# Optimization experiments

Hardware: AMD Instinct MI355X
Metric: run time of the kernel (lower is better)

The kernel has to match this reference:

```python
import jax, jax.numpy as jnp
import numpy as np

B, D, T = 16, 256, 4096
K = 1024
COMMITMENT_COST = 0.25


def setup_inputs() -> dict:
    key = jax.random.key(0)
    k1, k2 = jax.random.split(key)
    z = jax.random.normal(k1, (B, D, T), dtype=jnp.float32)
    # codebook initialized uniform(-1/K, 1/K) as in the torch module
    embeddings = jax.random.uniform(k2, (K, D), dtype=jnp.float32,
                                    minval=-1.0 / K, maxval=1.0 / K)
    return {"z": z, "embeddings": embeddings}


def reference(z, embeddings):
    # z: (B, D, T) -> (B, T, D)
    zt = jnp.transpose(z, (0, 2, 1))
    flat_z = zt.reshape(-1, D)  # (N, D), N = B*T
    # squared L2 distances to every codebook entry: (N, K)
    distances = (jnp.sum(flat_z * flat_z, axis=1, keepdims=True)
                 + jnp.sum(embeddings * embeddings, axis=1)
                 - 2.0 * flat_z @ embeddings.T)
    indices = jnp.argmin(distances, axis=1)  # (N,)
    # gather replaces the one-hot @ embeddings matmul (same result)
    quantized = embeddings[indices].reshape(B, T, D)
    # commitment loss (quantized detached)
    e_latent_loss = jnp.mean((jax.lax.stop_gradient(quantized) - zt) ** 2)
    loss = COMMITMENT_COST * e_latent_loss
    # straight-through estimator
    quantized_ste = zt + jax.lax.stop_gradient(quantized - zt)
    # perplexity from mean of one-hot encodings = normalized code histogram
    counts = jnp.zeros((K,), dtype=jnp.float32).at[indices].add(1.0)
    avg_probs = counts / flat_z.shape[0]
    perplexity = jnp.exp(-jnp.sum(avg_probs * jnp.log(avg_probs + 1e-10)))
    out = jnp.transpose(quantized_ste, (0, 2, 1))  # (B, D, T)
    return out, indices.reshape(B, T), loss, perplexity
```

## Files before the change

kernel.cpp:

```cpp
#include <hip/hip_runtime.h>
#include <hip/hip_bf16.h>

#define BB 16
#define DDIM 256
#define TLEN 4096
#define KCODES 1024
#define NQ (BB*TLEN)
#define QB 64
#define MAXC 32

#define FLT_MAX_C 3.402823466e+38f

using short8 = __attribute__((ext_vector_type(8))) short;
using f32x4  = __attribute__((ext_vector_type(4))) float;

__device__ __forceinline__ unsigned short f2bf(float x) {
  unsigned u = __float_as_uint(x);
  unsigned r = (u + 0x7fffu + ((u >> 16) & 1u)) >> 16;
  return (unsigned short)r;
}

__device__ __forceinline__ float np_sumsq_128(const float* q, int stride) {
  float r[8];
#pragma unroll
  for (int j = 0; j < 8; ++j) {
    float v = q[(size_t)j * (size_t)stride];
    r[j] = __fmul_rn(v, v);
  }
  for (int i = 8; i < 128; i += 8) {
#pragma unroll
    for (int j = 0; j < 8; ++j) {
      float v = q[(size_t)(i + j) * (size_t)stride];
      r[j] = __fadd_rn(r[j], __fmul_rn(v, v));
    }
  }
  return __fadd_rn(__fadd_rn(__fadd_rn(r[0], r[1]), __fadd_rn(r[2], r[3])),
                   __fadd_rn(__fadd_rn(r[4], r[5]), __fadd_rn(r[6], r[7])));
}
__device__ __forceinline__ float np_sumsq_256s(const float* p, int stride) {
  return __fadd_rn(np_sumsq_128(p, stride),
                   np_sumsq_128(p + (size_t)128 * stride, stride));
}

__global__ void k_prep(const float* __restrict__ emb, float* __restrict__ e2,
                       short* __restrict__ ebh, unsigned* __restrict__ maxe) {
  const int k = blockIdx.x;
  const int d = threadIdx.x;
  __shared__ float row[DDIM];
  float v = emb[(size_t)k * DDIM + d];
  row[d] = v;
  ebh[(size_t)k * DDIM + d] = (short)f2bf(v);
  float a = fabsf(v);
#pragma unroll
  for (int m = 1; m < 64; m <<= 1) a = fmaxf(a, __shfl_xor(a, m, 64));
  if ((threadIdx.x & 63) == 0) atomicMax(maxe, __float_as_uint(a));
  __syncthreads();
  if (d == 0) e2[k] = np_sumsq_256s(row, 1);
}

__global__ __launch_bounds__(512, 1)
void k_mdist(const float* __restrict__ z, const float* __restrict__ emb,
             const short* __restrict__ ebh, const float* __restrict__ e2,
             const unsigned* __restrict__ maxeU, float* __restrict__ out,
             float* __restrict__ oidx, int* __restrict__ hist,
             double* __restrict__ lossp) {
  extern __shared__ __align__(16) char sbuf[];
  float*  zf   = (float*)sbuf;
  short8* abh  = (short8*)(sbuf + 65536);
  float* bd    = (float*)(sbuf + 65536);
  int*   bk    = (int*)(sbuf + 65536 + 2048);
  float* sm    = (float*)(sbuf + 98304);
  float* qmin  = (float*)(sbuf + 98304 + 2048);
  int*   cand  = (int*)(sbuf + 98304 + 2304);
  int*   cnt   = (int*)(sbuf + 98304 + 10496);
  int*   ovf   = (int*)(sbuf + 98304 + 10752);
  float* z2s   = (float*)(sbuf + 98304 + 11008);
  float* sabs  = (float*)(sbuf + 98304 + 11264);
  int*   sidxs = (int*)(sbuf + 98304 + 11520);

  const int tid = threadIdx.x;
  const int lane = tid & 63;
  const int w = tid >> 6;
  const int g = lane >> 4;
  const int c = lane & 15;
  const int n0 = blockIdx.x * QB;
  const int b = n0 >> 12;
  const int t0 = n0 & (TLEN - 1);
  const float* zp = z + (size_t)b * DDIM * TLEN + t0;

#pragma unroll
  for (int i = 0; i < 8; ++i) {
    int s4 = i * 512 + tid;
    int dl = s4 >> 4, q4 = (s4 & 15) * 4;
    *(float4*)&zf[dl * QB + q4] = *(const float4*)(zp + (size_t)dl * TLEN + q4);
  }
  __syncthreads();

#pragma unroll
  for (int i = 0; i < 4; ++i) {
    int s = i * 512 + tid;
    int ks = s >> 8, mt = (s >> 6) & 3, ln = s & 63;
    int q = mt * 16 + (ln & 15);
    int d0 = ks * 32 + (ln >> 4) * 8;
    short8 hh;
#pragma unroll
    for (int j = 0; j < 8; ++j) hh[j] = (short)f2bf(zf[(d0 + j) * QB + q]);
    abh[s] = hh;
  }
  if (tid < QB) {
    z2s[tid] = np_sumsq_256s(&zf[tid], QB);
    float sa = 0.f;
    for (int d = 0; d < DDIM; ++d) sa += fabsf(zf[d * QB + tid]);
    sabs[tid] = sa;
    cnt[tid] = 0;
    ovf[tid] = 0;
  }
  __syncthreads();

  const float maxe = __uint_as_float(*maxeU);

#pragma unroll 1
  for (int h = 0; h < 2; ++h) {
    const int kb = h * 512 + w * 64;

    f32x4 acc[4][4];
#pragma unroll
    for (int mt = 0; mt < 4; ++mt)
#pragma unroll
      for (int nt = 0; nt < 4; ++nt) {
        f32x4 zz = {0.f, 0.f, 0.f, 0.f};
        acc[mt][nt] = zz;
      }

    const short* ebp = ebh + (size_t)(kb + c) * DDIM + g * 8;
    short8 bbuf[4];
#pragma unroll
    for (int nt = 0; nt < 4; ++nt)
      bbuf[nt] = *(const short8*)(ebp + nt * (16 * DDIM));

    for (int ks = 0; ks < 8; ++ks) {
      short8 ah[4];
#pragma unroll
      for (int mt = 0; mt < 4; ++mt) ah[mt] = abh[ks * 256 + mt * 64 + lane];
      const int ksn = (ks + 1) & 7;
#pragma unroll
      for (int nt = 0; nt < 4; ++nt) {
        short8 bv = bbuf[nt];
        bbuf[nt] = *(const short8*)(ebp + nt * (16 * DDIM) + ksn * 32);
#pragma unroll
        for (int mt = 0; mt < 4; ++mt)
          acc[mt][nt] = __builtin_amdgcn_mfma_f32_16x16x32_bf16(
              ah[mt], bv, acc[mt][nt], 0, 0, 0);
      }
    }

    float e2c[4];
#pragma unroll
    for (int nt = 0; nt < 4; ++nt) e2c[nt] = e2[kb + nt * 16 + c];

#pragma unroll
    for (int mt = 0; mt < 4; ++mt) {
      float m4[4];
#pragma unroll
      for (int r = 0; r < 4; ++r) {
        float m = FLT_MAX_C;
#pragma unroll
        for (int nt = 0; nt < 4; ++nt)
          m = fminf(m, e2c[nt] - 2.0f * acc[mt][nt][r]);
#pragma unroll
        for (int s = 1; s < 16; s <<= 1) m = fminf(m, __shfl_xor(m, s, 64));
        m4[r] = m;
      }
      if (c == 0) {
#pragma unroll
        for (int r = 0; r < 4; ++r) sm[w * 64 + mt * 16 + g * 4 + r] = m4[r];
      }
    }
    __syncthreads();
    if (tid < QB) {
      float m = sm[tid];
#pragma unroll
      for (int wv = 1; wv < 8; ++wv) m = fminf(m, sm[wv * 64 + tid]);
      qmin[tid] = m;
    }
    __syncthreads();

#pragma unroll
    for (int mt = 0; mt < 4; ++mt)
#pragma unroll
      for (int r = 0; r < 4; ++r) {
        const int ql = mt * 16 + g * 4 + r;
        const float lim = qmin[ql] + (maxe * sabs[ql]) * 0.016f + 2e-4f;
#pragma unroll
        for (int nt = 0; nt < 4; ++nt) {
          float s = e2c[nt] - 2.0f * acc[mt][nt][r];
          if (s <= lim) {
            int p = atomicAdd(&cnt[ql], 1);
            if (p < MAXC) cand[ql * MAXC + p] = kb + nt * 16 + c;
            else ovf[ql] = 1;
          }
        }
      }
    __syncthreads();
  }

  {
    const int q = tid & 63;
    const int slot = tid >> 6;
    const float z2q = z2s[q];
    float bestd = FLT_MAX_C;
    int besti = (1 << 30);
    const bool all = (ovf[q] != 0) || (cnt[q] > MAXC);
    const int count = all ? KCODES : cnt[q];
    for (int ci = slot; ci < count; ci += 8) {
      const int k = all ? ci : cand[q * MAXC + ci];
      const float4* ek = (const float4*)(emb + (size_t)k * DDIM);
      float a0 = 0.f;
      for (int dd = 0; dd < 64; ++dd) {
        float4 e4 = ek[dd];
        a0 = __fmaf_rn(zf[(dd * 4 + 0) * QB + q], e4.x, a0);
        a0 = __fmaf_rn(zf[(dd * 4 + 1) * QB + q], e4.y, a0);
        a0 = __fmaf_rn(zf[(dd * 4 + 2) * QB + q], e4.z, a0);
        a0 = __fmaf_rn(zf[(dd * 4 + 3) * QB + q], e4.w, a0);
      }
      float dist = __fsub_rn(__fadd_rn(z2q, e2[k]), __fmul_rn(2.0f, a0));
      if (dist < bestd || (dist == bestd && k < besti)) { bestd = dist; besti = k; }
    }
    bd[q * 8 + slot] = bestd;
    bk[q * 8 + slot] = besti;
  }
  __syncthreads();

  if (tid < QB) {
    float B = bd[tid * 8 + 0];
    int K = bk[tid * 8 + 0];
#pragma unroll
    for (int s = 1; s < 8; ++s) {
      float d2 = bd[tid * 8 + s];
      int k2 = bk[tid * 8 + s];
      if (d2 < B || (d2 == B && k2 < K)) { B = d2; K = k2; }
    }
    K &= (KCODES - 1);
    sidxs[tid] = K;
    oidx[n0 + tid] = (float)K;
    atomicAdd(&hist[K], 1);
    double ls = (double)B;
#pragma unroll
    for (int m = 1; m < 64; m <<= 1) ls += __shfl_xor(ls, m, 64);
    if (tid == 0) lossp[blockIdx.x] = ls;
  }
  __syncthreads();

  float* obase = out + (size_t)b * DDIM * TLEN + t0;
#pragma unroll
  for (int i = 0; i < 32; ++i) {
    int e = i * 512 + tid;
    int q = e & 63, d = e >> 6;
    obase[(size_t)d * TLEN + q] = emb[(size_t)sidxs[q] * DDIM + d];
  }
}

__global__ void k_final(const int* __restrict__ hist,
                        const double* __restrict__ lossp,
                        float* __restrict__ out2) {
  const int tid = threadIdx.x;
  double ls = 0.0;
  for (int i = 0; i < 4; ++i) ls += lossp[tid * 4 + i];
  float es = 0.f;
  for (int i = tid; i < KCODES; i += 256) {
    float p = (float)hist[i] / 65536.0f;
    es += p * logf(p + 1e-10f);
  }
#pragma unroll
  for (int m = 1; m < 64; m <<= 1) {
    ls += __shfl_xor(ls, m, 64);
    es += __shfl_xor(es, m, 64);
  }
  __shared__ double lw[4];
  __shared__ float ew[4];
  if ((tid & 63) == 0) { lw[tid >> 6] = ls; ew[tid >> 6] = es; }
  __syncthreads();
  if (tid == 0) {
    double lt = lw[0] + lw[1] + lw[2] + lw[3];
    float et = ew[0] + ew[1] + ew[2] + ew[3];
    float loss = 0.25f * (float)(lt / (double)((long long)NQ * DDIM));
    float perp = expf(-et);
    out2[0] = loss;
    out2[1] = perp;
  }
}

extern "C" void kernel_launch(void* const* d_in, const int* in_sizes, int n_in,
                              void* d_out, int out_size, void* d_ws, size_t ws_size,
                              hipStream_t stream) {
  const float* z = (const float*)d_in[0];
  const float* emb = (const float*)d_in[1];
  float* out = (float*)d_out;

  char* ws = (char*)d_ws;
  float* e2 = (float*)(ws);
  int* hist = (int*)(ws + 4096);
  unsigned* maxe = (unsigned*)(ws + 8192);
  double* lossp = (double*)(ws + 8200);
  short* ebh = (short*)(ws + 16400);

  float* oidx = out + ((size_t)out_size - 2 - NQ);
  float* out2 = out + ((size_t)out_size - 2);

  (void)hipFuncSetAttribute((const void*)k_mdist,
                            hipFuncAttributeMaxDynamicSharedMemorySize,
                            110080);

  hipMemsetAsync(hist, 0, 4100, stream);

  k_prep<<<KCODES, 256, 0, stream>>>(emb, e2, ebh, maxe);
  k_mdist<<<NQ / QB, 512, 110080, stream>>>(z, emb, ebh, e2, maxe, out, oidx,
                                            hist, lossp);
  k_final<<<1, 256, 0, stream>>>(hist, lossp, out2);
}
```

Baseline: 258.0 us.

## Split quantized-output gather into separate kernel and shrink distance kernel LDS

The distance kernel no longer keeps the full fp32 z tile in shared memory. It stages z in two 128-row halves and reads z from global memory for the exact fp32 rescoring. The output gather moves to a new kernel that holds a transposed codebook row in LDS and writes coalesced float4 output. The aim is to cut LDS use (from about 110KB to about 66KB) so two blocks can fit per CU, and to replace the uncoalesced per-element gather. The cost is an extra kernel launch, an index round-trip through global memory, and strided global reads of z during rescoring.

```diff
diff --git a/kernel.cpp b/kernel.cpp
--- a/kernel.cpp
+++ b/kernel.cpp
@@ -42,13 +42,15 @@
                    np_sumsq_128(p + (size_t)128 * stride, stride));
 }
 
-__global__ void k_prep(const float* __restrict__ emb, float* __restrict__ e2,
-                       short* __restrict__ ebh, unsigned* __restrict__ maxe) {
+__global__ void k_prep(const float* __restrict__ emb, float* __restrict__ embT,
+                       float* __restrict__ e2, short* __restrict__ ebh,
+                       unsigned* __restrict__ maxe) {
   const int k = blockIdx.x;
   const int d = threadIdx.x;
   __shared__ float row[DDIM];
   float v = emb[(size_t)k * DDIM + d];
   row[d] = v;
+  embT[(size_t)d * KCODES + k] = v;
   ebh[(size_t)k * DDIM + d] = (short)f2bf(v);
   float a = fabsf(v);
 #pragma unroll
@@ -61,22 +63,21 @@
 __global__ __launch_bounds__(512, 1)
 void k_mdist(const float* __restrict__ z, const float* __restrict__ emb,
              const short* __restrict__ ebh, const float* __restrict__ e2,
-             const unsigned* __restrict__ maxeU, float* __restrict__ out,
+             const unsigned* __restrict__ maxeU, int* __restrict__ idx,
              float* __restrict__ oidx, int* __restrict__ hist,
              double* __restrict__ lossp) {
   extern __shared__ __align__(16) char sbuf[];
-  float*  zf   = (float*)sbuf;
-  short8* abh  = (short8*)(sbuf + 65536);
-  float* bd    = (float*)(sbuf + 65536);
-  int*   bk    = (int*)(sbuf + 65536 + 2048);
-  float* sm    = (float*)(sbuf + 98304);
-  float* qmin  = (float*)(sbuf + 98304 + 2048);
-  int*   cand  = (int*)(sbuf + 98304 + 2304);
-  int*   cnt   = (int*)(sbuf + 98304 + 10496);
-  int*   ovf   = (int*)(sbuf + 98304 + 10752);
-  float* z2s   = (float*)(sbuf + 98304 + 11008);
-  float* sabs  = (float*)(sbuf + 98304 + 11264);
-  int*   sidxs = (int*)(sbuf + 98304 + 11520);
+  float*  zs   = (float*)sbuf;
+  float* sm    = (float*)sbuf;
+  float* qmin  = (float*)(sbuf + 2048);
+  int*   cand  = (int*)(sbuf + 4096);
+  float* bd    = (float*)(sbuf + 12288);
+  int*   bk    = (int*)(sbuf + 14336);
+  short8* abh  = (short8*)(sbuf + 32768);
+  float* z2s   = (float*)(sbuf + 65536);
+  float* sabs  = (float*)(sbuf + 65536 + 256);
+  int*   cnt   = (int*)(sbuf + 65536 + 512);
+  int*   ovf   = (int*)(sbuf + 65536 + 768);
 
   const int tid = threadIdx.x;
   const int lane = tid & 63;
@@ -88,40 +89,48 @@
   const int t0 = n0 & (TLEN - 1);
   const float* zp = z + (size_t)b * DDIM * TLEN + t0;
 
-#pragma unroll
-  for (int i = 0; i < 8; ++i) {
-    int s4 = i * 512 + tid;
-    int dl = s4 >> 4, q4 = (s4 & 15) * 4;
-    *(float4*)&zf[dl * QB + q4] = *(const float4*)(zp + (size_t)dl * TLEN + q4);
-  }
-  __syncthreads();
-
-#pragma unroll
-  for (int i = 0; i < 4; ++i) {
-    int s = i * 512 + tid;
-    int ks = s >> 8, mt = (s >> 6) & 3, ln = s & 63;
-    int q = mt * 16 + (ln & 15);
-    int d0 = ks * 32 + (ln >> 4) * 8;
-    short8 hh;
-#pragma unroll
-    for (int j = 0; j < 8; ++j) hh[j] = (short)f2bf(zf[(d0 + j) * QB + q]);
-    abh[s] = hh;
-  }
-  if (tid < QB) {
-    z2s[tid] = np_sumsq_256s(&zf[tid], QB);
-    float sa = 0.f;
-    for (int d = 0; d < DDIM; ++d) sa += fabsf(zf[d * QB + tid]);
-    sabs[tid] = sa;
-    cnt[tid] = 0;
-    ovf[tid] = 0;
-  }
-  __syncthreads();
+  float th0 = 0.f, sa0 = 0.f;
+#pragma unroll
+  for (int h = 0; h < 2; ++h) {
+#pragma unroll
+    for (int i = 0; i < 4; ++i) {
+      int s4 = i * 512 + tid;
+      int dl = s4 >> 4, q4 = (s4 & 15) * 4;
+      *(float4*)&zs[dl * QB + q4] =
+          *(const float4*)(zp + (size_t)(h * 128 + dl) * TLEN + q4);
+    }
+    __syncthreads();
+#pragma unroll
+    for (int i = 0; i < 2; ++i) {
+      int s = i * 512 + tid;
+      int ksl = s >> 8, mt = (s >> 6) & 3, ln = s & 63;
+      int q = mt * 16 + (ln & 15);
+      int d0l = ksl * 32 + (ln >> 4) * 8;
+      short8 hh;
+#pragma unroll
+      for (int j = 0; j < 8; ++j) hh[j] = (short)f2bf(zs[(d0l + j) * QB + q]);
+      abh[(h * 4 + ksl) * 256 + mt * 64 + ln] = hh;
+    }
+    if (tid < QB) {
+      float th = np_sumsq_128(&zs[tid], QB);
+      float sa = 0.f;
+      for (int d = 0; d < 128; ++d) sa += fabsf(zs[d * QB + tid]);
+      if (h == 0) {
+        th0 = th; sa0 = sa;
+        cnt[tid] = 0; ovf[tid] = 0;
+      } else {
+        z2s[tid] = __fadd_rn(th0, th);
+        sabs[tid] = sa0 + sa;
+      }
+    }
+    __syncthreads();
+  }
 
   const float maxe = __uint_as_float(*maxeU);
 
 #pragma unroll 1
-  for (int h = 0; h < 2; ++h) {
-    const int kb = h * 512 + w * 64;
+  for (int ch = 0; ch < 2; ++ch) {
+    const int kb = ch * 512 + w * 64;
 
     f32x4 acc[4][4];
 #pragma unroll
@@ -208,21 +217,17 @@
     const int q = tid & 63;
     const int slot = tid >> 6;
     const float z2q = z2s[q];
+    const float* zq = zp + q;
     float bestd = FLT_MAX_C;
     int besti = (1 << 30);
     const bool all = (ovf[q] != 0) || (cnt[q] > MAXC);
     const int count = all ? KCODES : cnt[q];
     for (int ci = slot; ci < count; ci += 8) {
       const int k = all ? ci : cand[q * MAXC + ci];
-      const float4* ek = (const float4*)(emb + (size_t)k * DDIM);
+      const float* ek = emb + (size_t)k * DDIM;
       float a0 = 0.f;
-      for (int dd = 0; dd < 64; ++dd) {
-        float4 e4 = ek[dd];
-        a0 = __fmaf_rn(zf[(dd * 4 + 0) * QB + q], e4.x, a0);
-        a0 = __fmaf_rn(zf[(dd * 4 + 1) * QB + q], e4.y, a0);
-        a0 = __fmaf_rn(zf[(dd * 4 + 2) * QB + q], e4.z, a0);
-        a0 = __fmaf_rn(zf[(dd * 4 + 3) * QB + q], e4.w, a0);
-      }
+      for (int d = 0; d < DDIM; ++d)
+        a0 = __fmaf_rn(zq[(size_t)d * TLEN], ek[d], a0);
       float dist = __fsub_rn(__fadd_rn(z2q, e2[k]), __fmul_rn(2.0f, a0));
       if (dist < bestd || (dist == bestd && k < besti)) { bestd = dist; besti = k; }
     }
@@ -241,7 +246,7 @@
       if (d2 < B || (d2 == B && k2 < K)) { B = d2; K = k2; }
     }
     K &= (KCODES - 1);
-    sidxs[tid] = K;
+    idx[n0 + tid] = K;
     oidx[n0 + tid] = (float)K;
     atomicAdd(&hist[K], 1);
     double ls = (double)B;
@@ -249,14 +254,31 @@
     for (int m = 1; m < 64; m <<= 1) ls += __shfl_xor(ls, m, 64);
     if (tid == 0) lossp[blockIdx.x] = ls;
   }
+}
+
+__global__ void k_gather(const float* __restrict__ embT,
+                         const int* __restrict__ idx,
+                         float* __restrict__ out) {
+  __shared__ float er[KCODES];
+  const int blk = blockIdx.x;
+  const int bq = blk >> 8;
+  const int d = blk & 255;
+  const int tid = threadIdx.x;
+  *((float4*)&er[tid * 4]) =
+      *((const float4*)(embT + (size_t)d * KCODES + tid * 4));
   __syncthreads();
-
-  float* obase = out + (size_t)b * DDIM * TLEN + t0;
-#pragma unroll
-  for (int i = 0; i < 32; ++i) {
-    int e = i * 512 + tid;
-    int q = e & 63, d = e >> 6;
-    obase[(size_t)d * TLEN + q] = emb[(size_t)sidxs[q] * DDIM + d];
+  const int* ip = idx + (size_t)bq * TLEN;
+  float* op = out + (size_t)blk * TLEN;
+#pragma unroll
+  for (int cch = 0; cch < 4; ++cch) {
+    int t0 = cch * 1024 + tid * 4;
+    int4 ii = *(const int4*)&ip[t0];
+    float4 v;
+    v.x = er[ii.x & (KCODES - 1)];
+    v.y = er[ii.y & (KCODES - 1)];
+    v.z = er[ii.z & (KCODES - 1)];
+    v.w = er[ii.w & (KCODES - 1)];
+    *(float4*)&op[t0] = v;
   }
 }
 
@@ -298,23 +320,26 @@
   float* out = (float*)d_out;
 
   char* ws = (char*)d_ws;
-  float* e2 = (float*)(ws);
-  int* hist = (int*)(ws + 4096);
-  unsigned* maxe = (unsigned*)(ws + 8192);
-  double* lossp = (double*)(ws + 8200);
-  short* ebh = (short*)(ws + 16400);
+  float* embT = (float*)(ws);
+  float* e2 = (float*)(ws + 1048576);
+  int* hist = (int*)(ws + 1052672);
+  unsigned* maxe = (unsigned*)(ws + 1056768);
+  double* lossp = (double*)(ws + 1056776);
+  int* idx = (int*)(ws + 1064968);
+  short* ebh = (short*)(ws + 1327112);
 
   float* oidx = out + ((size_t)out_size - 2 - NQ);
   float* out2 = out + ((size_t)out_size - 2);
 
   (void)hipFuncSetAttribute((const void*)k_mdist,
                             hipFuncAttributeMaxDynamicSharedMemorySize,
-                            110080);
+                            66560);
 
   hipMemsetAsync(hist, 0, 4100, stream);
 
-  k_prep<<<KCODES, 256, 0, stream>>>(emb, e2, ebh, maxe);
-  k_mdist<<<NQ / QB, 512, 110080, stream>>>(z, emb, ebh, e2, maxe, out, oidx,
-                                            hist, lossp);
+  k_prep<<<KCODES, 256, 0, stream>>>(emb, embT, e2, ebh, maxe);
+  k_mdist<<<NQ / QB, 512, 66560, stream>>>(z, emb, ebh, e2, maxe, idx, oidx,
+                                           hist, lossp);
+  k_gather<<<BB * DDIM, 256, 0, stream>>>(embT, idx, out);
   k_final<<<1, 256, 0, stream>>>(hist, lossp, out2);
 }
```

New measurement: 268.8 us. +4.2%, slower.
